# Performance work log

Measured on AMD Instinct MI355X. Metric: run time of the kernel, lower is better.

## Reference

```python
import jax, jax.numpy as jnp
import numpy as np

B, T, D = 2, 2048, 2048
H, KV = 16, 4
HD = D // H           # head_dim = 128
G = H // KV           # group size = 4
VOCAB = 32000


def setup_inputs() -> dict:
    key = jax.random.key(0)
    k1, k2, k3, k4, k5, k6 = jax.random.split(key, 6)
    hidden_state = jax.random.normal(k1, (B, T, D), dtype=jnp.float32)
    ids = jax.random.randint(k2, (B, T), 1, VOCAB)  # avoid pad id 0
    ids = ids.at[:, T - T // 8:].set(0)             # trailing padding
    inputs_id = ids.astype(jnp.int64)
    s = 1.0 / np.sqrt(D)
    Wq = jax.random.normal(k3, (D, H * HD), dtype=jnp.float32) * s
    Wk = jax.random.normal(k4, (D, KV * HD), dtype=jnp.float32) * s
    Wv = jax.random.normal(k5, (D, KV * HD), dtype=jnp.float32) * s
    Wo = jax.random.normal(k6, (H * HD, D), dtype=jnp.float32) * s
    return {"hidden_state": hidden_state, "inputs_id": inputs_id,
            "Wq": Wq, "Wk": Wk, "Wv": Wv, "Wo": Wo}


def reference(hidden_state, inputs_id, Wq, Wk, Wv, Wo):
    b, t = inputs_id.shape
    # masks: padding over KEYS, combined with causal
    pad = (inputs_id != 0)[:, None, None, :]                 # [B,1,1,T]
    causal = jnp.tril(jnp.ones((t, t), dtype=bool))[None, None]  # [1,1,T,T]
    mask = pad & causal                                       # [B,1,T,T]

    q = (hidden_state @ Wq).reshape(b, t, H, HD).transpose(0, 2, 1, 3)  # [B,H,T,hd]
    k = (hidden_state @ Wk).reshape(b, t, KV, HD)
    v = (hidden_state @ Wv).reshape(b, t, KV, HD)
    # faithful to torch expand/reshape: head h -> kv head (h % KV)
    k = jnp.broadcast_to(k[:, :, None], (b, t, G, KV, HD)).reshape(b, t, H, HD).transpose(0, 2, 1, 3)
    v = jnp.broadcast_to(v[:, :, None], (b, t, G, KV, HD)).reshape(b, t, H, HD).transpose(0, 2, 1, 3)

    scores = jnp.einsum('bhqd,bhkd->bhqk', q, k) / np.sqrt(HD)
    scores = jnp.where(mask, scores, -jnp.inf)
    probs = jax.nn.softmax(scores, axis=-1)
    out = jnp.einsum('bhqk,bhkd->bhqd', probs, v)             # [B,H,T,hd]
    out = out.transpose(0, 2, 1, 3).reshape(b, t, H * HD)
    return out @ Wo
```

## Files before the change

### kernel.cpp

```cpp
#include <hip/hip_runtime.h>

#define B_ 2
#define T_ 2048
#define D_ 2048
#define H_ 16
#define KV_ 4
#define HD_ 128
#define M_ (B_*T_)

typedef __attribute__((ext_vector_type(8))) short s8v;
typedef __attribute__((ext_vector_type(4))) float f4v;
typedef __attribute__((ext_vector_type(16))) float f16v;
typedef __attribute__((ext_vector_type(8))) __bf16 b8v;
typedef __attribute__((ext_vector_type(4))) unsigned u4v;

__device__ __forceinline__ short f2bs(float f) {
  unsigned u = __builtin_bit_cast(unsigned, f);
  u += 0x7fffu + ((u >> 16) & 1u);
  return (short)(u >> 16);
}
__device__ __forceinline__ void plswap2(unsigned &x, unsigned &y) {
  asm volatile("v_permlane32_swap_b32 %0, %1" : "+v"(x), "+v"(y));
}
__device__ __forceinline__ unsigned cvtpk(float lo, float hi) {
  unsigned r;
  asm("v_cvt_pk_bf16_f32 %0, %1, %2" : "=v"(r) : "v"(lo), "v"(hi));
  return r;
}

__global__ void prep_kernel(const float* __restrict__ hs,
                            const float* __restrict__ Wq, const float* __restrict__ Wk,
                            const float* __restrict__ Wv, const float* __restrict__ Wo,
                            short* __restrict__ hsb,
                            short* __restrict__ WT, short* __restrict__ WoT) {
  int bid = blockIdx.x;
  const int tid = threadIdx.y * 32 + threadIdx.x;
  if (bid >= 10240) {
    const int i = (bid - 10240) * 256 + tid;
    float4 v = reinterpret_cast<const float4*>(hs)[i];
    short4 o;
    o.x = f2bs(v.x); o.y = f2bs(v.y); o.z = f2bs(v.z); o.w = f2bs(v.w);
    reinterpret_cast<short4*>(hsb)[i] = o;
    return;
  }
  __shared__ float t[32][33];
  const float* W; short* dst; int N, rowoff;
  if (bid < 4096)      { W = Wq; dst = WT;  N = 2048; rowoff = 0;    }
  else if (bid < 5120) { W = Wk; dst = WT;  N = 512;  rowoff = 2048; bid -= 4096; }
  else if (bid < 6144) { W = Wv; dst = WT;  N = 512;  rowoff = 2560; bid -= 5120; }
  else                 { W = Wo; dst = WoT; N = 2048; rowoff = 0;    bid -= 6144; }
  const int nbl = N >> 5;
  const int nb = (bid % nbl) * 32, kb = (bid / nbl) * 32;
  const int tx = threadIdx.x, ty = threadIdx.y;
#pragma unroll
  for (int j = 0; j < 4; ++j)
    t[ty + j*8][tx] = W[(size_t)(kb + ty + j*8) * N + nb + tx];
  __syncthreads();
#pragma unroll
  for (int j = 0; j < 4; ++j)
    dst[(size_t)(rowoff + nb + ty + j*8) * 2048 + kb + tx] = f2bs(t[tx][ty + j*8]);
}

template<int MODE>
__global__ __launch_bounds__(256) void gemm_bt_kernel(const short* __restrict__ A,
                                                      const short* __restrict__ BT,
                                                      void* __restrict__ Cv,
                                                      short* __restrict__ Kv,
                                                      short* __restrict__ Vt,
                                                      int M, int N, int K) {
  __shared__ alignas(16) short As[3][128*32];
  __shared__ alignas(16) short Bs[3][128*32];
  const int tid  = threadIdx.x;
  const int wave = tid >> 6;
  const int lane = tid & 63;
  const int lr = lane & 15;
  const int lk = (lane >> 4) * 8;
  const int m0 = blockIdx.y * 128;
  const int n0 = blockIdx.x * 128;
  const int wr = (wave >> 1) * 64;
  const int wc = (wave & 1) * 64;

  const int srow = tid >> 2, skc = tid & 3;
  const short* gaBase  = A  + (size_t)(m0 + srow) * K + skc*8;
  const short* gbBase  = BT + (size_t)(n0 + srow) * K + skc*8;
  const short* gaBase2 = A  + (size_t)(m0 + 64 + srow) * K + skc*8;
  const short* gbBase2 = BT + (size_t)(n0 + 64 + srow) * K + skc*8;
  const int ldsOff  = (wave*64) * 8;
  const int ldsOff2 = (256 + wave*64) * 8;

  f4v acc[4][4];
#pragma unroll
  for (int m = 0; m < 4; ++m)
#pragma unroll
    for (int n = 0; n < 4; ++n) acc[m][n] = (f4v)0.0f;

  auto STAGE = [&](int tile, int slot) {
    const int kn = tile * 32;
    short* a1 = &As[slot][0];
    short* b1 = &Bs[slot][0];
    __builtin_amdgcn_global_load_lds((const __attribute__((address_space(1))) void*)(gaBase + kn),
        (__attribute__((address_space(3))) void*)(a1 + ldsOff), 16, 0, 0);
    __builtin_amdgcn_global_load_lds((const __attribute__((address_space(1))) void*)(gbBase + kn),
        (__attribute__((address_space(3))) void*)(b1 + ldsOff), 16, 0, 0);
    __builtin_amdgcn_global_load_lds((const __attribute__((address_space(1))) void*)(gaBase2 + kn),
        (__attribute__((address_space(3))) void*)(a1 + ldsOff2), 16, 0, 0);
    __builtin_amdgcn_global_load_lds((const __attribute__((address_space(1))) void*)(gbBase2 + kn),
        (__attribute__((address_space(3))) void*)(b1 + ldsOff2), 16, 0, 0);
  };

  const int NT = K >> 5;
  STAGE(0, 0);
  STAGE(1, 1);
  asm volatile("s_waitcnt vmcnt(4)" ::: "memory");
  __builtin_amdgcn_s_barrier();
  __builtin_amdgcn_sched_barrier(0);

  for (int t = 0; t < NT; ++t) {
    if (t + 2 < NT) STAGE(t + 2, (t + 2) % 3);
    const short* Ac = &As[t % 3][0];
    const short* Bc = &Bs[t % 3][0];
    s8v af[4], bfv[4];
#pragma unroll
    for (int m = 0; m < 4; ++m)
      af[m] = *reinterpret_cast<const s8v*>(Ac + (wr + m*16 + lr)*32 + lk);
#pragma unroll
    for (int n = 0; n < 4; ++n)
      bfv[n] = *reinterpret_cast<const s8v*>(Bc + (wc + n*16 + lr)*32 + lk);
#pragma unroll
    for (int m = 0; m < 4; ++m)
#pragma unroll
      for (int n = 0; n < 4; ++n)
        acc[m][n] = __builtin_amdgcn_mfma_f32_16x16x32_bf16(
            __builtin_bit_cast(b8v, af[m]), __builtin_bit_cast(b8v, bfv[n]),
            acc[m][n], 0, 0, 0);
    if (t + 1 < NT) {
      if (t < NT - 2) { asm volatile("s_waitcnt vmcnt(4)" ::: "memory"); }
      else            { asm volatile("s_waitcnt vmcnt(0)" ::: "memory"); }
      __builtin_amdgcn_s_barrier();
      __builtin_amdgcn_sched_barrier(0);
    }
  }

  if (MODE == 3 && n0 >= 2560) {
#pragma unroll
    for (int m = 0; m < 4; ++m) {
#pragma unroll
      for (int n = 0; n < 4; ++n) {
        const int col = n0 + wc + n*16 + lr - 2560;
        const int row = m0 + wr + m*16 + (lane >> 4)*4;
        short4 o;
        o.x = f2bs(acc[m][n][0]); o.y = f2bs(acc[m][n][1]);
        o.z = f2bs(acc[m][n][2]); o.w = f2bs(acc[m][n][3]);
        *reinterpret_cast<short4*>(Vt + (size_t)col * M + row) = o;
      }
    }
  } else {
#pragma unroll
    for (int m = 0; m < 4; ++m) {
#pragma unroll
      for (int n = 0; n < 4; ++n) {
#pragma unroll
        for (int i = 0; i < 4; ++i) {
          const int row = m0 + wr + m*16 + (lane >> 4)*4 + i;
          const int col = n0 + wc + n*16 + lr;
          if (MODE == 1)
            reinterpret_cast<float*>(Cv)[(size_t)row * N + col] = acc[m][n][i];
          else if (col < 2048)
            reinterpret_cast<short*>(Cv)[(size_t)row * 2048 + col] = f2bs(acc[m][n][i]);
          else
            Kv[(size_t)row * 512 + (col - 2048)] = f2bs(acc[m][n][i]);
        }
      }
    }
  }
}

__device__ __forceinline__ void stage_tile(short* KsBuf, short* VtBuf,
                                           const short* __restrict__ Kb,
                                           const short* __restrict__ Vtg,
                                           int bT, int kv0, int kvh,
                                           int tid, int wave) {
#pragma unroll
  for (int j = 0; j < 4; ++j) {
    const int f = j*256 + tid;
    const int row = f >> 4, cd = f & 15, cs = cd ^ (row & 7);
    const short* g = Kb + (size_t)(bT + kv0 + row)*512 + kvh*HD_ + cs*8;
    short* l = KsBuf + (j*256 + wave*64) * 8;
    __builtin_amdgcn_global_load_lds((const __attribute__((address_space(1))) void*)g,
                                     (__attribute__((address_space(3))) void*)l, 16, 0, 0);
  }
#pragma unroll
  for (int j = 0; j < 4; ++j) {
    const int f = j*256 + tid;
    const int d = f >> 3, cd = f & 7, cs = cd ^ (d & 7);
    const short* g = Vtg + (size_t)(kvh*HD_ + d)*M_ + bT + kv0 + cs*8;
    short* l = VtBuf + (j*256 + wave*64) * 8;
    __builtin_amdgcn_global_load_lds((const __attribute__((address_space(1))) void*)g,
                                     (__attribute__((address_space(3))) void*)l, 16, 0, 0);
  }
}

__global__ __launch_bounds__(256, 2) void attn_kernel(const short* __restrict__ Q,
                                                      const short* __restrict__ Kb,
                                                      const short* __restrict__ Vtg,
                                                      const int* __restrict__ ids,
                                                      short* __restrict__ AO) {
  __shared__ alignas(16) short Ks[2][64*128];
  __shared__ alignas(16) short Vt[2][128*64];

  const int bid = blockIdx.x;
  const int g   = bid & 31;
  const int gr  = bid >> 5;
  const int p   = (gr < 8) ? (15 - gr) : (gr - 8);
  const int h   = g & (H_-1);
  const int b   = g >> 4;
  const int kvh = h & (KV_-1);
  const int tid = threadIdx.x;
  const int wq  = tid >> 6;
  const int lane = tid & 63;
  const int ql  = lane & 31;
  const int hi  = lane >> 5;
  const int bT  = b * T_;
  const int q0  = p * 128;
  const int qrow = q0 + wq*32 + ql;
  const int nt  = 2*(p+1);
  const float SC = 0.08838834764831845f * 1.4426950408889634f;

  s8v qf[8];
  const size_t qgbase = (size_t)(bT + qrow) * (H_*HD_) + h*HD_;
#pragma unroll
  for (int mm = 0; mm < 8; ++mm)
    qf[mm] = *reinterpret_cast<const s8v*>(Q + qgbase + mm*16 + hi*8);

  f16v oacc[4];
#pragma unroll
  for (int n = 0; n < 4; ++n) oacc[n] = (f16v)0.0f;
  float m_run = -1.0e30f, lsum = 0.0f;

  stage_tile(Ks[0], Vt[0], Kb, Vtg, bT, 0, kvh, tid, wq);
  int cur = 0;
  for (int t = 0; t < nt; ++t) {
    __syncthreads();
    if (t + 1 < nt)
      stage_tile(Ks[cur^1], Vt[cur^1], Kb, Vtg, bT, (t+1)*64, kvh, tid, wq);
    const int kv0 = t * 64;
    const char* KsC = reinterpret_cast<const char*>(Ks[cur]);
    const char* VtC = reinterpret_cast<const char*>(Vt[cur]);

    const unsigned long long pmask = __ballot(ids[bT + kv0 + lane] != 0);

    f16v sacc[2];
    sacc[0] = (f16v)0.0f; sacc[1] = (f16v)0.0f;
#pragma unroll
    for (int mm = 0; mm < 8; ++mm) {
#pragma unroll
      for (int kb = 0; kb < 2; ++kb) {
        const int row = kb*32 + ql;
        s8v kf = *reinterpret_cast<const s8v*>(KsC +
            ((row*256 + mm*32 + hi*16) ^ ((row & 7) << 4)));
        sacc[kb] = __builtin_amdgcn_mfma_f32_32x32x16_bf16(
            __builtin_bit_cast(b8v, kf), __builtin_bit_cast(b8v, qf[mm]), sacc[kb], 0, 0, 0);
      }
    }

    float tm[16];
#pragma unroll
    for (int r = 0; r < 16; ++r) tm[r] = fmaxf(sacc[0][r], sacc[1][r]);
#pragma unroll
    for (int r = 0; r < 8; ++r) tm[r] = fmaxf(tm[r], tm[r+8]);
#pragma unroll
    for (int r = 0; r < 4; ++r) tm[r] = fmaxf(tm[r], tm[r+4]);
    tm[0] = fmaxf(fmaxf(tm[0], tm[1]), fmaxf(tm[2], tm[3]));
    const float mx = fmaxf(tm[0], __shfl_xor(tm[0], 32));

    if (!__all(mx <= m_run + 20.0f)) {
      const float mn = fmaxf(m_run, mx);
      const float corr = exp2f((m_run - mn) * SC);
      lsum *= corr;
#pragma unroll
      for (int n = 0; n < 4; ++n)
#pragma unroll
        for (int r = 0; r < 16; ++r) oacc[n][r] *= corr;
      m_run = mn;
    }
    const float nm = -m_run * SC;
    const bool fast = (kv0 + 63 <= q0 + wq*32) && (pmask == ~0ull);

    float psum = 0.0f;
#pragma unroll
    for (int kb = 0; kb < 2; ++kb) {
      float pv[16];
#pragma unroll
      for (int r = 0; r < 16; ++r)
        pv[r] = exp2f(fmaf(sacc[kb][r], SC, nm));
      if (!fast) {
        const int th = qrow - kv0 - kb*32 - 4*hi;
        const unsigned cw = (th >= 28) ? 0xffffffffu
                          : ((th < 0) ? 0u : ((2u << th) - 1u));
        const unsigned vm = cw & (unsigned)(pmask >> (kb*32 + 4*hi));
#pragma unroll
        for (int r = 0; r < 16; ++r) {
          const int C = (r & 3) + 8*(r >> 2);
          pv[r] = ((vm >> C) & 1u) ? pv[r] : 0.0f;
        }
      }
      float ps[8];
#pragma unroll
      for (int r = 0; r < 8; ++r) ps[r] = pv[r] + pv[r+8];
#pragma unroll
      for (int r = 0; r < 4; ++r) ps[r] += ps[r+4];
      psum += (ps[0] + ps[1]) + (ps[2] + ps[3]);

      unsigned pa = cvtpk(pv[0],  pv[1]),  pb = cvtpk(pv[2],  pv[3]);
      unsigned pc = cvtpk(pv[4],  pv[5]),  pd = cvtpk(pv[6],  pv[7]);
      unsigned pe = cvtpk(pv[8],  pv[9]),  pf_ = cvtpk(pv[10], pv[11]);
      unsigned pg = cvtpk(pv[12], pv[13]), ph = cvtpk(pv[14], pv[15]);
      plswap2(pa, pc);  plswap2(pb, pd);
      plswap2(pe, pg);  plswap2(pf_, ph);
      u4v pw0 = {pa, pb, pc, pd};
      u4v pw1 = {pe, pf_, pg, ph};

#pragma unroll
      for (int s = 0; s < 2; ++s) {
        const b8v pf = __builtin_bit_cast(b8v, s ? pw1 : pw0);
        const int ks = 2*kb + s;
#pragma unroll
        for (int n = 0; n < 4; ++n) {
          const int d = n*32 + ql;
          s8v vf = *reinterpret_cast<const s8v*>(VtC +
              ((d*128 + ks*32 + hi*16) ^ ((d & 7) << 4)));
          oacc[n] = __builtin_amdgcn_mfma_f32_32x32x16_bf16(
              __builtin_bit_cast(b8v, vf), pf, oacc[n], 0, 0, 0);
        }
      }
    }
    lsum += psum + __shfl_xor(psum, 32);
    cur ^= 1;
  }

  const float inv = 1.0f / fmaxf(lsum, 1.0e-37f);
  const size_t obase = (size_t)(bT + qrow) * (H_*HD_) + h*HD_;
#pragma unroll
  for (int n = 0; n < 4; ++n) {
#pragma unroll
    for (int j = 0; j < 4; ++j) {
      short4 o;
      o.x = f2bs(oacc[n][4*j+0] * inv);
      o.y = f2bs(oacc[n][4*j+1] * inv);
      o.z = f2bs(oacc[n][4*j+2] * inv);
      o.w = f2bs(oacc[n][4*j+3] * inv);
      *reinterpret_cast<short4*>(AO + obase + n*32 + 8*j + 4*hi) = o;
    }
  }
}

extern "C" void kernel_launch(void* const* d_in, const int* in_sizes, int n_in,
                              void* d_out, int out_size, void* d_ws, size_t ws_size,
                              hipStream_t stream) {
  const float* hs = (const float*)d_in[0];
  const int*  ids = (const int*)d_in[1];
  const float* Wq = (const float*)d_in[2];
  const float* Wk = (const float*)d_in[3];
  const float* Wv = (const float*)d_in[4];
  const float* Wo = (const float*)d_in[5];
  char* ws = (char*)d_ws;

  short* hsb = (short*)(ws);
  short* WT  = (short*)(ws + (16u << 20));
  short* WoT = (short*)(ws + (28u << 20));
  short* Qb  = (short*)(ws + (36u << 20));
  short* Kb  = (short*)(ws + (52u << 20));
  short* Vtg = (short*)(ws + (56u << 20));
  short* AO  = hsb;
  float* out = (float*)d_out;

  prep_kernel<<<dim3(18432), dim3(32, 8), 0, stream>>>(hs, Wq, Wk, Wv, Wo, hsb, WT, WoT);

  gemm_bt_kernel<3><<<dim3(3072/128, 4096/128), dim3(256), 0, stream>>>(
      hsb, WT, Qb, Kb, Vtg, 4096, 3072, 2048);

  attn_kernel<<<dim3(512), dim3(256), 0, stream>>>(Qb, Kb, Vtg, ids, AO);

  gemm_bt_kernel<1><<<dim3(2048/128, 4096/128), dim3(256), 0, stream>>>(
      AO, WoT, out, nullptr, nullptr, 4096, 2048, 2048);
}
```

Before: 212.6 us.

## Split long causal attention query tiles across two blocks and merge with combine kernel

The five longest query tiles (p=11..15) are now split into two KV-range halves, each handled by its own block. The blocks write unnormalized bf16 partial outputs plus per-row max and sum into a scratch buffer that reuses the weight workspace. A new combine kernel merges each pair using log-sum-exp weights. Block order is rearranged to balance the 256-CU load by starting long work early. The cost is an extra kernel launch, scratch traffic, and extra bf16 rounding of the partial outputs.

```diff
diff --git a/kernel.cpp b/kernel.cpp
--- a/kernel.cpp
+++ b/kernel.cpp
@@ -18,6 +18,10 @@
   unsigned u = __builtin_bit_cast(unsigned, f);
   u += 0x7fffu + ((u >> 16) & 1u);
   return (short)(u >> 16);
+}
+__device__ __forceinline__ float bs2f(short s) {
+  unsigned u = ((unsigned)(unsigned short)s) << 16;
+  return __builtin_bit_cast(float, u);
 }
 __device__ __forceinline__ void plswap2(unsigned &x, unsigned &y) {
   asm volatile("v_permlane32_swap_b32 %0, %1" : "+v"(x), "+v"(y));
@@ -200,21 +204,45 @@
   }
 }
 
+#define PHALF 33792
+#define PGI   67584
+
 __global__ __launch_bounds__(256, 2) void attn_kernel(const short* __restrict__ Q,
                                                       const short* __restrict__ Kb,
                                                       const short* __restrict__ Vtg,
                                                       const int* __restrict__ ids,
-                                                      short* __restrict__ AO) {
+                                                      short* __restrict__ AO,
+                                                      char* __restrict__ pbuf) {
   __shared__ alignas(16) short Ks[2][64*128];
   __shared__ alignas(16) short Vt[2][128*64];
 
   const int bid = blockIdx.x;
-  const int g   = bid & 31;
-  const int gr  = bid >> 5;
-  const int p   = (gr < 8) ? (15 - gr) : (gr - 8);
-  const int h   = g & (H_-1);
-  const int b   = g >> 4;
+  int p, bh, split = 0, half = 0, r;
+  if      (bid <  32) { p = 10; bh = bid;       }
+  else if (bid <  64) { p = 9;  bh = bid - 32;  }
+  else if (bid <  96) { p = 8;  bh = bid - 64;  }
+  else if (bid < 160) { p = 15; r = bid - 96;  bh = r >> 1; half = r & 1; split = 1; }
+  else if (bid < 192) { p = 7;  bh = bid - 160; }
+  else if (bid < 256) { p = 14; r = bid - 192; bh = r >> 1; half = r & 1; split = 1; }
+  else if (bid < 320) { p = 13; r = bid - 256; bh = r >> 1; half = r & 1; split = 1; }
+  else if (bid < 352) { p = 6;  bh = bid - 320; }
+  else if (bid < 416) { p = 12; r = bid - 352; bh = r >> 1; half = r & 1; split = 1; }
+  else if (bid < 448) { p = 5;  bh = bid - 416; }
+  else if (bid < 512) { p = 11; r = bid - 448; bh = r >> 1; half = r & 1; split = 1; }
+  else if (bid < 544) { p = 4;  bh = bid - 512; }
+  else if (bid < 576) { p = 3;  bh = bid - 544; }
+  else if (bid < 608) { p = 2;  bh = bid - 576; }
+  else if (bid < 640) { p = 1;  bh = bid - 608; }
+  else                { p = 0;  bh = bid - 640; }
+
+  const int h   = bh & (H_-1);
+  const int b   = bh >> 4;
   const int kvh = h & (KV_-1);
+  const int nt  = 2*(p+1);
+  const int ht  = p + 1;
+  const int t0  = (split && half) ? ht : 0;
+  const int t1  = split ? (half ? nt : ht) : nt;
+
   const int tid = threadIdx.x;
   const int wq  = tid >> 6;
   const int lane = tid & 63;
@@ -223,7 +251,6 @@
   const int bT  = b * T_;
   const int q0  = p * 128;
   const int qrow = q0 + wq*32 + ql;
-  const int nt  = 2*(p+1);
   const float SC = 0.08838834764831845f * 1.4426950408889634f;
 
   s8v qf[8];
@@ -237,11 +264,11 @@
   for (int n = 0; n < 4; ++n) oacc[n] = (f16v)0.0f;
   float m_run = -1.0e30f, lsum = 0.0f;
 
-  stage_tile(Ks[0], Vt[0], Kb, Vtg, bT, 0, kvh, tid, wq);
+  stage_tile(Ks[0], Vt[0], Kb, Vtg, bT, t0*64, kvh, tid, wq);
   int cur = 0;
-  for (int t = 0; t < nt; ++t) {
+  for (int t = t0; t < t1; ++t) {
     __syncthreads();
-    if (t + 1 < nt)
+    if (t + 1 < t1)
       stage_tile(Ks[cur^1], Vt[cur^1], Kb, Vtg, bT, (t+1)*64, kvh, tid, wq);
     const int kv0 = t * 64;
     const char* KsC = reinterpret_cast<const char*>(Ks[cur]);
@@ -265,11 +292,11 @@
 
     float tm[16];
 #pragma unroll
-    for (int r = 0; r < 16; ++r) tm[r] = fmaxf(sacc[0][r], sacc[1][r]);
-#pragma unroll
-    for (int r = 0; r < 8; ++r) tm[r] = fmaxf(tm[r], tm[r+8]);
-#pragma unroll
-    for (int r = 0; r < 4; ++r) tm[r] = fmaxf(tm[r], tm[r+4]);
+    for (int rr = 0; rr < 16; ++rr) tm[rr] = fmaxf(sacc[0][rr], sacc[1][rr]);
+#pragma unroll
+    for (int rr = 0; rr < 8; ++rr) tm[rr] = fmaxf(tm[rr], tm[rr+8]);
+#pragma unroll
+    for (int rr = 0; rr < 4; ++rr) tm[rr] = fmaxf(tm[rr], tm[rr+4]);
     tm[0] = fmaxf(fmaxf(tm[0], tm[1]), fmaxf(tm[2], tm[3]));
     const float mx = fmaxf(tm[0], __shfl_xor(tm[0], 32));
 
@@ -280,7 +307,7 @@
 #pragma unroll
       for (int n = 0; n < 4; ++n)
 #pragma unroll
-        for (int r = 0; r < 16; ++r) oacc[n][r] *= corr;
+        for (int rr = 0; rr < 16; ++rr) oacc[n][rr] *= corr;
       m_run = mn;
     }
     const float nm = -m_run * SC;
@@ -291,24 +318,24 @@
     for (int kb = 0; kb < 2; ++kb) {
       float pv[16];
 #pragma unroll
-      for (int r = 0; r < 16; ++r)
-        pv[r] = exp2f(fmaf(sacc[kb][r], SC, nm));
+      for (int rr = 0; rr < 16; ++rr)
+        pv[rr] = exp2f(fmaf(sacc[kb][rr], SC, nm));
       if (!fast) {
         const int th = qrow - kv0 - kb*32 - 4*hi;
         const unsigned cw = (th >= 28) ? 0xffffffffu
                           : ((th < 0) ? 0u : ((2u << th) - 1u));
         const unsigned vm = cw & (unsigned)(pmask >> (kb*32 + 4*hi));
 #pragma unroll
-        for (int r = 0; r < 16; ++r) {
-          const int C = (r & 3) + 8*(r >> 2);
-          pv[r] = ((vm >> C) & 1u) ? pv[r] : 0.0f;
+        for (int rr = 0; rr < 16; ++rr) {
+          const int C = (rr & 3) + 8*(rr >> 2);
+          pv[rr] = ((vm >> C) & 1u) ? pv[rr] : 0.0f;
         }
       }
       float ps[8];
 #pragma unroll
-      for (int r = 0; r < 8; ++r) ps[r] = pv[r] + pv[r+8];
-#pragma unroll
-      for (int r = 0; r < 4; ++r) ps[r] += ps[r+4];
+      for (int rr = 0; rr < 8; ++rr) ps[rr] = pv[rr] + pv[rr+8];
+#pragma unroll
+      for (int rr = 0; rr < 4; ++rr) ps[rr] += ps[rr+4];
       psum += (ps[0] + ps[1]) + (ps[2] + ps[3]);
 
       unsigned pa = cvtpk(pv[0],  pv[1]),  pb = cvtpk(pv[2],  pv[3]);
@@ -338,19 +365,75 @@
     cur ^= 1;
   }
 
-  const float inv = 1.0f / fmaxf(lsum, 1.0e-37f);
-  const size_t obase = (size_t)(bT + qrow) * (H_*HD_) + h*HD_;
-#pragma unroll
-  for (int n = 0; n < 4; ++n) {
-#pragma unroll
-    for (int j = 0; j < 4; ++j) {
-      short4 o;
-      o.x = f2bs(oacc[n][4*j+0] * inv);
-      o.y = f2bs(oacc[n][4*j+1] * inv);
-      o.z = f2bs(oacc[n][4*j+2] * inv);
-      o.w = f2bs(oacc[n][4*j+3] * inv);
-      *reinterpret_cast<short4*>(AO + obase + n*32 + 8*j + 4*hi) = o;
-    }
+  if (!split) {
+    const float inv = 1.0f / fmaxf(lsum, 1.0e-37f);
+    const size_t obase = (size_t)(bT + qrow) * (H_*HD_) + h*HD_;
+#pragma unroll
+    for (int n = 0; n < 4; ++n) {
+#pragma unroll
+      for (int j = 0; j < 4; ++j) {
+        short4 o;
+        o.x = f2bs(oacc[n][4*j+0] * inv);
+        o.y = f2bs(oacc[n][4*j+1] * inv);
+        o.z = f2bs(oacc[n][4*j+2] * inv);
+        o.w = f2bs(oacc[n][4*j+3] * inv);
+        *reinterpret_cast<short4*>(AO + obase + n*32 + 8*j + 4*hi) = o;
+      }
+    }
+  } else {
+    char* pg = pbuf + (size_t)(bh*5 + (p - 11)) * PGI + half * PHALF;
+    short* pO = (short*)pg;
+    float* pM = (float*)(pg + 32768);
+    float* pL = (float*)(pg + 33280);
+    const int row = wq*32 + ql;
+#pragma unroll
+    for (int n = 0; n < 4; ++n) {
+#pragma unroll
+      for (int j = 0; j < 4; ++j) {
+        short4 o;
+        o.x = f2bs(oacc[n][4*j+0]);
+        o.y = f2bs(oacc[n][4*j+1]);
+        o.z = f2bs(oacc[n][4*j+2]);
+        o.w = f2bs(oacc[n][4*j+3]);
+        *reinterpret_cast<short4*>(pO + row*128 + n*32 + 8*j + 4*hi) = o;
+      }
+    }
+    if (hi == 0) { pM[row] = m_run; pL[row] = lsum; }
+  }
+}
+
+__global__ __launch_bounds__(256) void combine_kernel(const char* __restrict__ pbuf,
+                                                      short* __restrict__ AO) {
+  const int gi = blockIdx.x;
+  const int bh = gi / 5, pp = gi % 5, p = 11 + pp;
+  const int h = bh & (H_-1), b = bh >> 4;
+  const char* g0 = pbuf + (size_t)gi * PGI;
+  const char* g1 = g0 + PHALF;
+  const int t = threadIdx.x;
+  const int row = t >> 1, dh = (t & 1) * 64;
+  const float SC = 0.08838834764831845f * 1.4426950408889634f;
+
+  const float m1 = ((const float*)(g0 + 32768))[row];
+  const float l1 = ((const float*)(g0 + 33280))[row];
+  const float m2 = ((const float*)(g1 + 32768))[row];
+  const float l2 = ((const float*)(g1 + 33280))[row];
+  const float m  = fmaxf(m1, m2);
+  const float w1 = exp2f((m1 - m) * SC);
+  const float w2 = exp2f((m2 - m) * SC);
+  const float inv = 1.0f / fmaxf(w1*l1 + w2*l2, 1.0e-37f);
+
+  const short* O1 = (const short*)g0 + row*128 + dh;
+  const short* O2 = (const short*)g1 + row*128 + dh;
+  short* dst = AO + (size_t)(b*T_ + p*128 + row) * (H_*HD_) + h*HD_ + dh;
+#pragma unroll
+  for (int c = 0; c < 8; ++c) {
+    s8v a = *reinterpret_cast<const s8v*>(O1 + c*8);
+    s8v v = *reinterpret_cast<const s8v*>(O2 + c*8);
+    s8v o;
+#pragma unroll
+    for (int e = 0; e < 8; ++e)
+      o[e] = f2bs((w1 * bs2f(a[e]) + w2 * bs2f(v[e])) * inv);
+    *reinterpret_cast<s8v*>(dst + c*8) = o;
   }
 }
 
@@ -372,6 +455,7 @@
   short* Kb  = (short*)(ws + (52u << 20));
   short* Vtg = (short*)(ws + (56u << 20));
   short* AO  = hsb;
+  char*  pbuf = (char*)WT;
   float* out = (float*)d_out;
 
   prep_kernel<<<dim3(18432), dim3(32, 8), 0, stream>>>(hs, Wq, Wk, Wv, Wo, hsb, WT, WoT);
@@ -379,7 +463,8 @@
   gemm_bt_kernel<3><<<dim3(3072/128, 4096/128), dim3(256), 0, stream>>>(
       hsb, WT, Qb, Kb, Vtg, 4096, 3072, 2048);
 
-  attn_kernel<<<dim3(512), dim3(256), 0, stream>>>(Qb, Kb, Vtg, ids, AO);
+  attn_kernel<<<dim3(672), dim3(256), 0, stream>>>(Qb, Kb, Vtg, ids, AO, pbuf);
+  combine_kernel<<<dim3(160), dim3(256), 0, stream>>>(pbuf, AO);
 
   gemm_bt_kernel<1><<<dim3(2048/128, 4096/128), dim3(256), 0, stream>>>(
       AO, WoT, out, nullptr, nullptr, 4096, 2048, 2048);
```

Result: no change. 214.6 us (+0.9%).
